# Performance work log

Hardware: AMD Instinct MI355X
Metric: run time of the kernel (lower is better)

Reference implementation:

```python
import jax, jax.numpy as jnp
import numpy as np

B, C, D, N, K = 2, 64, 3, 4096, 16
E = 2 * C      # edge-feature channels (128)
H = 2 * E      # expansion hidden channels (256)


def setup_inputs() -> dict:
    key = jax.random.key(0)
    ks = jax.random.split(key, 7)
    s1 = 1.0 / np.sqrt(E).astype(np.float32)
    s2 = 1.0 / np.sqrt(H).astype(np.float32)
    return {
        "x":  jax.random.normal(ks[0], (B, C, D, N), jnp.float32),
        "W1": jax.random.normal(ks[1], (H, E), jnp.float32) * s1,
        "b1": jax.random.normal(ks[2], (H,), jnp.float32) * s1,
        "W2": jax.random.normal(ks[3], (H, H), jnp.float32) * s2,
        "b2": jax.random.normal(ks[4], (H,), jnp.float32) * s2,
        "W3": jax.random.normal(ks[5], (C, H), jnp.float32) * s2,
        "b3": jax.random.normal(ks[6], (C,), jnp.float32) * s2,
    }


def _knn_idx(pc, k):
    """pc: (B, C, N). Returns (B, k, N) indices of k nearest neighbors
    (self excluded), matching KNN(ref=pc, query=pc) then idx[:, 1:, :]."""
    sq = jnp.sum(pc * pc, axis=1)                                  # (B, N)
    d2 = sq[:, :, None] - 2.0 * jnp.einsum('bcn,bcm->bnm', pc, pc) + sq[:, None, :]
    _, idx = jax.lax.top_k(-d2, k + 1)                             # (B, N, k+1) nearest-first
    return jnp.transpose(idx[:, :, 1:], (0, 2, 1))                 # drop self -> (B, k, N)


def reference(x, W1, b1, W2, b2, W3, b3):
    mean_pc = jnp.mean(x, axis=2)                                  # (B, C, N)
    idx = _knn_idx(mean_pc, K)                                     # (B, K, N), int32
    # grouping_operation: out[b,c,k,n] = mean_pc[b, c, idx[b,k,n]]
    nbr = jax.vmap(lambda f, i: f[:, i])(mean_pc, idx)             # (B, C, K, N)
    central = jnp.broadcast_to(x[:, :, None, :, :], (B, C, K, D, N))
    nbr_e = jnp.broadcast_to(nbr[:, :, :, None, :], (B, C, K, D, N))
    edge = jnp.concatenate([central, nbr_e - central], axis=1)     # (B, 2C, K, D, N)
    bc = lambda b: b[None, :, None, None, None]
    h = jax.nn.relu(jnp.einsum('oi,bikdn->bokdn', W1, edge) + bc(b1))
    h = jax.nn.relu(jnp.einsum('oi,bikdn->bokdn', W2, h) + bc(b2))
    r = jnp.einsum('oi,bikdn->bokdn', W3, h) + bc(b3)              # (B, C, K, D, N)
    return jnp.max(r, axis=2) + x                                  # (B, C, D, N)
```

## Files before the change

kernel.cpp:

```cpp
#include <hip/hip_runtime.h>

typedef unsigned short u16;
typedef float f32x4 __attribute__((ext_vector_type(4)));
typedef short bf16x8 __attribute__((ext_vector_type(8)));
typedef u16 u16x4 __attribute__((ext_vector_type(4)));
typedef unsigned int uint2v __attribute__((ext_vector_type(2)));


static __device__ __forceinline__ u16 f2bf(float x) {
    union { float f; unsigned int u; } v; v.f = x;
    unsigned int u = v.u;
    unsigned int r = u + 0x7fffu + ((u >> 16) & 1u);
    return (u16)(r >> 16);
}

static __device__ __forceinline__ float bf2f(u16 h) {
    union { unsigned int u; float f; } v; v.u = ((unsigned int)h) << 16;
    return v.f;
}

static __device__ __forceinline__ unsigned int pk2(float a, float b) {
    return (unsigned int)f2bf(a) | ((unsigned int)f2bf(b) << 16);
}

__global__ __launch_bounds__(256) void mean_kernel(const float* __restrict__ x,
                                                   float* __restrict__ pc) {
    int t = blockIdx.x * 256 + threadIdx.x;
    int n = t & 4095;
    int bc = t >> 12;
    const float* xp = x + bc * 3 * 4096 + n;
    pc[t] = (xp[0] + xp[4096] + xp[8192]) / 3.0f;
}

__global__ __launch_bounds__(256) void sq_kernel(const float* __restrict__ pc,
                                                 float* __restrict__ sq) {
    int t = blockIdx.x * 256 + threadIdx.x;
    int b = t >> 12, n = t & 4095;
    float s = 0.f;
    #pragma unroll
    for (int c = 0; c < 64; ++c) {
        float v = pc[(b * 64 + c) * 4096 + n];
        s += v * v;
    }
    sq[t] = s;
}

#define INSERT(dist, idxv) do { \
    float _v = (dist); int _vi = (idxv); \
    _Pragma("unroll") \
    for (int _s = 0; _s < 16; ++_s) { \
        bool _c = _v < bd[_s]; \
        float _nb = _c ? _v : bd[_s]; \
        float _nv = _c ? bd[_s] : _v; \
        int _nbi = _c ? _vi : bi[_s]; \
        int _nvi = _c ? bi[_s] : _vi; \
        bd[_s] = _nb; _v = _nv; bi[_s] = _nbi; _vi = _nvi; \
    } } while (0)

__global__ __launch_bounds__(256, 3) void knn_part_kernel(const float* __restrict__ pc,
                                                          const float* __restrict__ sq,
                                                          float* __restrict__ pd,
                                                          int* __restrict__ pi) {
    __shared__ float ptile[64][128];
    __shared__ float sqt[128];
    int tid = threadIdx.x;
    int bid = blockIdx.x;
    int ch = bid & 31, qb = (bid >> 5) & 15, b = bid >> 9;
    int n = qb * 256 + tid;
    int m0 = ch * 128;

    #pragma unroll
    for (int it = 0; it < 8; ++it) {
        int lin4 = it * 256 + tid;
        int c = lin4 >> 5, mm4 = (lin4 & 31) * 4;
        *(float4*)&ptile[c][mm4] =
            *(const float4*)&pc[(b * 64 + c) * 4096 + m0 + mm4];
    }
    if (tid < 128) sqt[tid] = sq[b * 4096 + m0 + tid];

    float qv[64];
    #pragma unroll
    for (int c = 0; c < 64; ++c) qv[c] = pc[(b * 64 + c) * 4096 + n];
    float sqn = sq[b * 4096 + n];

    float bd[16]; int bi[16];
    #pragma unroll
    for (int s = 0; s < 16; ++s) { bd[s] = 3.4e38f; bi[s] = -1; }
    __syncthreads();

    for (int mb = 0; mb < 128; mb += 4) {
        float d0 = 0.f, d1 = 0.f, d2 = 0.f, d3 = 0.f;
        #pragma unroll
        for (int c = 0; c < 64; ++c) {
            float4 pv = *(const float4*)&ptile[c][mb];
            float qc = qv[c];
            d0 = fmaf(qc, pv.x, d0);
            d1 = fmaf(qc, pv.y, d1);
            d2 = fmaf(qc, pv.z, d2);
            d3 = fmaf(qc, pv.w, d3);
        }
        int m = m0 + mb;
        float e0 = (sqn - 2.f * d0) + sqt[mb + 0]; if (m + 0 == n) e0 = 3.4e38f;
        float e1 = (sqn - 2.f * d1) + sqt[mb + 1]; if (m + 1 == n) e1 = 3.4e38f;
        float e2 = (sqn - 2.f * d2) + sqt[mb + 2]; if (m + 2 == n) e2 = 3.4e38f;
        float e3 = (sqn - 2.f * d3) + sqt[mb + 3]; if (m + 3 == n) e3 = 3.4e38f;
        INSERT(e0, m + 0);
        INSERT(e1, m + 1);
        INSERT(e2, m + 2);
        INSERT(e3, m + 3);
    }
    int base = ((b * 4096 + n) * 32 + ch) * 16;
    #pragma unroll
    for (int s = 0; s < 16; ++s) { pd[base + s] = bd[s]; pi[base + s] = bi[s]; }
}

__global__ __launch_bounds__(256) void knn_merge_kernel(const float* __restrict__ pd,
                                                        const int* __restrict__ pi,
                                                        int* __restrict__ idxw) {
    int tid = threadIdx.x;
    int lane = tid & 63;
    int q = blockIdx.x * 4 + (tid >> 6);
    int base = q * 512;

    float d[8]; int ix[8];
    #pragma unroll
    for (int j = 0; j < 8; ++j) {
        d[j] = pd[base + lane + 64 * j];
        ix[j] = pi[base + lane + 64 * j];
    }

    for (int e = 0; e < 16; ++e) {
        float lmd = d[0]; int lmi = ix[0];
        #pragma unroll
        for (int j = 1; j < 8; ++j) {
            bool c = d[j] < lmd;
            lmd = c ? d[j] : lmd;
            lmi = c ? ix[j] : lmi;
        }
        float wm = lmd;
        #pragma unroll
        for (int off = 32; off; off >>= 1)
            wm = fminf(wm, __shfl_xor(wm, off));
        unsigned long long msk = __ballot(lmd == wm);
        int L = (int)__ffsll(msk) - 1;
        int wmi = __shfl(lmi, L);
        if (lane == 0) idxw[q * 16 + e] = wmi;
        if (lane == L) {
            #pragma unroll
            for (int j = 0; j < 8; ++j)
                if (ix[j] == wmi) d[j] = 3.4e38f;
        }
    }
}

__global__ __launch_bounds__(256) void prep_kernel(const float* __restrict__ W1,
                                                   const float* __restrict__ W2,
                                                   const float* __restrict__ W3,
                                                   u16* __restrict__ W2bf,
                                                   u16* __restrict__ W3bf,
                                                   float* __restrict__ W1dT,
                                                   float* __restrict__ W1bT) {
    int t = blockIdx.x * 256 + threadIdx.x;
    W2bf[t] = f2bf(W2[t]);
    if (t < 16384) {
        W3bf[t] = f2bf(W3[t]);
        int c = t >> 8, h = t & 255;
        float wa = W1[h * 128 + c];
        float wb = W1[h * 128 + 64 + c];
        W1dT[t] = wa - wb;
        W1bT[t] = wb;
    }
}

__global__ __launch_bounds__(256) void q_kernel(const float* __restrict__ pc,
                                               const float* __restrict__ W1bT,
                                               u16* __restrict__ Qbf) {
    int h = threadIdx.x;
    int bid = blockIdx.x;
    int b = bid >> 10, m0 = (bid & 1023) * 4;
    float a0 = 0.f, a1 = 0.f, a2 = 0.f, a3 = 0.f;
    for (int c = 0; c < 64; ++c) {
        float w = W1bT[c * 256 + h];
        float4 pv = *(const float4*)(pc + (b * 64 + c) * 4096 + m0);
        a0 = fmaf(w, pv.x, a0);
        a1 = fmaf(w, pv.y, a1);
        a2 = fmaf(w, pv.z, a2);
        a3 = fmaf(w, pv.w, a3);
    }
    int ob = (b * 4096 + m0) * 256 + h;
    Qbf[ob] = f2bf(a0); Qbf[ob + 256] = f2bf(a1);
    Qbf[ob + 512] = f2bf(a2); Qbf[ob + 768] = f2bf(a3);
}

__global__ __launch_bounds__(256) void p_kernel(const float* __restrict__ x,
                                               const float* __restrict__ W1dT,
                                               const float* __restrict__ b1,
                                               u16* __restrict__ Pbf) {
    int h = threadIdx.x;
    int bid = blockIdx.x;
    int b = bid / 3072;
    int rem = bid % 3072;
    int d = rem >> 10;
    int n0 = (rem & 1023) * 4;
    float bias = b1[h];
    float a0 = bias, a1 = bias, a2 = bias, a3 = bias;
    for (int c = 0; c < 64; ++c) {
        float w = W1dT[c * 256 + h];
        float4 xv = *(const float4*)(x + ((b * 64 + c) * 3 + d) * 4096 + n0);
        a0 = fmaf(w, xv.x, a0);
        a1 = fmaf(w, xv.y, a1);
        a2 = fmaf(w, xv.z, a2);
        a3 = fmaf(w, xv.w, a3);
    }
    int ob = ((b * 3 + d) * 4096 + n0) * 256 + h;
    Pbf[ob] = f2bf(a0); Pbf[ob + 256] = f2bf(a1);
    Pbf[ob + 512] = f2bf(a2); Pbf[ob + 768] = f2bf(a3);
}

__global__ __launch_bounds__(256) void fused_mlp_kernel(const float* __restrict__ x,
                                                        const u16* __restrict__ Pbf,
                                                        const u16* __restrict__ Qbf,
                                                        const int* __restrict__ idxw,
                                                        const u16* __restrict__ W2bf,
                                                        const u16* __restrict__ W3bf,
                                                        const float* __restrict__ b2,
                                                        const float* __restrict__ b3,
                                                        float* __restrict__ out) {
    __shared__ u16 hL[96][264];

    int tid = threadIdx.x;
    int bid = blockIdx.x;
    int b = bid >> 11;
    int n0 = (bid & 2047) * 2;

    int w = tid >> 6, lane = tid & 63;

    {
        int g = w & 1, kh = (w >> 1) * 8;
        int n = n0 + g;
        u16x4 pv[3];
        #pragma unroll
        for (int d = 0; d < 3; ++d)
            pv[d] = *(const u16x4*)&Pbf[((b * 3 + d) * 4096 + n) * 256 + lane * 4];
        const int* idq = idxw + (b * 4096 + n) * 16 + kh;
        #pragma unroll
        for (int kk = 0; kk < 8; ++kk) {
            int m = idq[kk];
            u16x4 qv = *(const u16x4*)&Qbf[(b * 4096 + m) * 256 + lane * 4];
            float q0 = bf2f(qv[0]), q1 = bf2f(qv[1]), q2 = bf2f(qv[2]), q3 = bf2f(qv[3]);
            #pragma unroll
            for (int d = 0; d < 3; ++d) {
                uint2v hv;
                hv[0] = pk2(fmaxf(bf2f(pv[d][0]) + q0, 0.f), fmaxf(bf2f(pv[d][1]) + q1, 0.f));
                hv[1] = pk2(fmaxf(bf2f(pv[d][2]) + q2, 0.f), fmaxf(bf2f(pv[d][3]) + q3, 0.f));
                *(uint2v*)&hL[g * 48 + d * 16 + kh + kk][lane * 4] = hv;
            }
        }
    }
    __syncthreads();

    int cl = lane & 15, q = lane >> 4;

    f32x4 acc[4][6];
    #pragma unroll
    for (int i = 0; i < 4; ++i)
        #pragma unroll
        for (int jt = 0; jt < 6; ++jt)
            acc[i][jt] = (f32x4){0.f, 0.f, 0.f, 0.f};

    const u16* Arow = W2bf + (w * 64 + cl) * 256 + q * 8;
    for (int kt = 0; kt < 8; ++kt) {
        int k0 = kt * 32;
        bf16x8 a[4], bb[6];
        #pragma unroll
        for (int i = 0; i < 4; ++i)
            a[i] = *(const bf16x8*)(Arow + i * 4096 + k0);
        #pragma unroll
        for (int jt = 0; jt < 6; ++jt)
            bb[jt] = *(const bf16x8*)(&hL[jt * 16 + cl][k0 + q * 8]);
        #pragma unroll
        for (int i = 0; i < 4; ++i)
            #pragma unroll
            for (int jt = 0; jt < 6; ++jt)
                acc[i][jt] = __builtin_amdgcn_mfma_f32_16x16x32_bf16(a[i], bb[jt], acc[i][jt], 0, 0, 0);
    }
    __syncthreads();

    #pragma unroll
    for (int i = 0; i < 4; ++i) {
        int rowb = w * 64 + i * 16 + q * 4;
        float4 bv = *(const float4*)(b2 + rowb);
        #pragma unroll
        for (int jt = 0; jt < 6; ++jt) {
            f32x4 v = acc[i][jt];
            uint2v hv;
            hv[0] = pk2(fmaxf(v[0] + bv.x, 0.f), fmaxf(v[1] + bv.y, 0.f));
            hv[1] = pk2(fmaxf(v[2] + bv.z, 0.f), fmaxf(v[3] + bv.w, 0.f));
            *(uint2v*)&hL[jt * 16 + cl][rowb] = hv;
        }
    }
    __syncthreads();

    f32x4 acc3[6];
    #pragma unroll
    for (int jt = 0; jt < 6; ++jt) acc3[jt] = (f32x4){0.f, 0.f, 0.f, 0.f};

    const u16* A3row = W3bf + (w * 16 + cl) * 256 + q * 8;
    for (int kt = 0; kt < 8; ++kt) {
        int k0 = kt * 32;
        bf16x8 a3 = *(const bf16x8*)(A3row + k0);
        #pragma unroll
        for (int jt = 0; jt < 6; ++jt) {
            bf16x8 bb = *(const bf16x8*)(&hL[jt * 16 + cl][k0 + q * 8]);
            acc3[jt] = __builtin_amdgcn_mfma_f32_16x16x32_bf16(a3, bb, acc3[jt], 0, 0, 0);
        }
    }

    int rowb = w * 16 + q * 4;
    float4 b3v = *(const float4*)(b3 + rowb);
    #pragma unroll
    for (int jt = 0; jt < 6; ++jt) {
        int g = jt / 3, d = jt % 3;
        int n = n0 + g;
        f32x4 v = acc3[jt];
        v[0] += b3v.x;
        v[1] += b3v.y;
        v[2] += b3v.z;
        v[3] += b3v.w;
        #pragma unroll
        for (int off = 1; off < 16; off <<= 1) {
            v[0] = fmaxf(v[0], __shfl_xor(v[0], off));
            v[1] = fmaxf(v[1], __shfl_xor(v[1], off));
            v[2] = fmaxf(v[2], __shfl_xor(v[2], off));
            v[3] = fmaxf(v[3], __shfl_xor(v[3], off));
        }
        if (cl == 0) {
            #pragma unroll
            for (int r = 0; r < 4; ++r) {
                int addr = ((b * 64 + rowb + r) * 3 + d) * 4096 + n;
                out[addr] = v[r] + x[addr];
            }
        }
    }
}

extern "C" void kernel_launch(void* const* d_in, const int* in_sizes, int n_in,
                              void* d_out, int out_size, void* d_ws, size_t ws_size,
                              hipStream_t stream) {
    (void)in_sizes; (void)n_in; (void)out_size; (void)ws_size;
    const float* x  = (const float*)d_in[0];
    const float* W1 = (const float*)d_in[1];
    const float* b1 = (const float*)d_in[2];
    const float* W2 = (const float*)d_in[3];
    const float* b2 = (const float*)d_in[4];
    const float* W3 = (const float*)d_in[5];
    const float* b3 = (const float*)d_in[6];
    float* out = (float*)d_out;

    char* ws = (char*)d_ws;
    float* pc   = (float*)(ws + 0);
    float* sq   = (float*)(ws + 2097152);
    int*   idxw = (int*)  (ws + 2129920);
    u16*   Qbf  = (u16*)  (ws + 2654208);
    u16*   Pbf  = (u16*)  (ws + 6848512);
    u16*   W2bf = (u16*)  (ws + 19431424);
    u16*   W3bf = (u16*)  (ws + 19562496);
    float* W1dT = (float*)(ws + 19595264);
    float* W1bT = (float*)(ws + 19660800);
    float* pd   = (float*)(ws + 2654208);
    int*   pi   = (int*)  (ws + 19726336);

    mean_kernel<<<2048, 256, 0, stream>>>(x, pc);
    sq_kernel<<<32, 256, 0, stream>>>(pc, sq);
    knn_part_kernel<<<1024, 256, 0, stream>>>(pc, sq, pd, pi);
    knn_merge_kernel<<<2048, 256, 0, stream>>>(pd, pi, idxw);
    prep_kernel<<<256, 256, 0, stream>>>(W1, W2, W3, W2bf, W3bf, W1dT, W1bT);
    q_kernel<<<2048, 256, 0, stream>>>(pc, W1bT, Qbf);
    p_kernel<<<6144, 256, 0, stream>>>(x, W1dT, b1, Pbf);
    fused_mlp_kernel<<<4096, 256, 0, stream>>>(x, Pbf, Qbf, idxw, W2bf, W3bf, b2, b3, out);
}
```

Before: 379.0 us.

## Fuse weight prep into mean kernel, widen P/Q kernels, halve fused MLP LDS

Weight conversion moves into mean_kernel, which removes one launch. The q and p kernels now compute 8 points per block instead of 4, halving their grid sizes. fused_mlp_kernel processes its two points one after another, so the shared buffer shrinks to 48 rows and the accumulators halve. It also declares 4 waves-per-EU launch bounds to raise occupancy. In exchange, the W2/W3 fragments are reloaded per point and extra barriers are added.

```diff
diff --git a/kernel.cpp b/kernel.cpp
--- a/kernel.cpp
+++ b/kernel.cpp
@@ -5,6 +5,7 @@
 typedef short bf16x8 __attribute__((ext_vector_type(8)));
 typedef u16 u16x4 __attribute__((ext_vector_type(4)));
 typedef unsigned int uint2v __attribute__((ext_vector_type(2)));
+typedef unsigned int uint4v __attribute__((ext_vector_type(4)));
 
 
 static __device__ __forceinline__ u16 f2bf(float x) {
@@ -24,12 +25,31 @@
 }
 
 __global__ __launch_bounds__(256) void mean_kernel(const float* __restrict__ x,
-                                                   float* __restrict__ pc) {
+                                                   float* __restrict__ pc,
+                                                   const float* __restrict__ W1,
+                                                   const float* __restrict__ W2,
+                                                   const float* __restrict__ W3,
+                                                   u16* __restrict__ W2bf,
+                                                   u16* __restrict__ W3bf,
+                                                   float* __restrict__ W1dT,
+                                                   float* __restrict__ W1bT) {
     int t = blockIdx.x * 256 + threadIdx.x;
     int n = t & 4095;
     int bc = t >> 12;
     const float* xp = x + bc * 3 * 4096 + n;
     pc[t] = (xp[0] + xp[4096] + xp[8192]) / 3.0f;
+
+    if (t < 65536) {
+        W2bf[t] = f2bf(W2[t]);
+        if (t < 16384) {
+            W3bf[t] = f2bf(W3[t]);
+            int c = t >> 8, h = t & 255;
+            float wa = W1[h * 128 + c];
+            float wb = W1[h * 128 + 64 + c];
+            W1dT[t] = wa - wb;
+            W1bT[t] = wb;
+        }
+    }
 }
 
 __global__ __launch_bounds__(256) void sq_kernel(const float* __restrict__ pc,
@@ -153,43 +173,29 @@
     }
 }
 
-__global__ __launch_bounds__(256) void prep_kernel(const float* __restrict__ W1,
-                                                   const float* __restrict__ W2,
-                                                   const float* __restrict__ W3,
-                                                   u16* __restrict__ W2bf,
-                                                   u16* __restrict__ W3bf,
-                                                   float* __restrict__ W1dT,
-                                                   float* __restrict__ W1bT) {
-    int t = blockIdx.x * 256 + threadIdx.x;
-    W2bf[t] = f2bf(W2[t]);
-    if (t < 16384) {
-        W3bf[t] = f2bf(W3[t]);
-        int c = t >> 8, h = t & 255;
-        float wa = W1[h * 128 + c];
-        float wb = W1[h * 128 + 64 + c];
-        W1dT[t] = wa - wb;
-        W1bT[t] = wb;
-    }
-}
-
 __global__ __launch_bounds__(256) void q_kernel(const float* __restrict__ pc,
                                                const float* __restrict__ W1bT,
                                                u16* __restrict__ Qbf) {
     int h = threadIdx.x;
     int bid = blockIdx.x;
-    int b = bid >> 10, m0 = (bid & 1023) * 4;
+    int b = bid >> 9, m0 = (bid & 511) * 8;
     float a0 = 0.f, a1 = 0.f, a2 = 0.f, a3 = 0.f;
+    float a4 = 0.f, a5 = 0.f, a6 = 0.f, a7 = 0.f;
     for (int c = 0; c < 64; ++c) {
         float w = W1bT[c * 256 + h];
-        float4 pv = *(const float4*)(pc + (b * 64 + c) * 4096 + m0);
-        a0 = fmaf(w, pv.x, a0);
-        a1 = fmaf(w, pv.y, a1);
-        a2 = fmaf(w, pv.z, a2);
-        a3 = fmaf(w, pv.w, a3);
+        const float* pr = pc + (b * 64 + c) * 4096 + m0;
+        float4 p0 = *(const float4*)pr;
+        float4 p1 = *(const float4*)(pr + 4);
+        a0 = fmaf(w, p0.x, a0); a1 = fmaf(w, p0.y, a1);
+        a2 = fmaf(w, p0.z, a2); a3 = fmaf(w, p0.w, a3);
+        a4 = fmaf(w, p1.x, a4); a5 = fmaf(w, p1.y, a5);
+        a6 = fmaf(w, p1.z, a6); a7 = fmaf(w, p1.w, a7);
     }
     int ob = (b * 4096 + m0) * 256 + h;
     Qbf[ob] = f2bf(a0); Qbf[ob + 256] = f2bf(a1);
     Qbf[ob + 512] = f2bf(a2); Qbf[ob + 768] = f2bf(a3);
+    Qbf[ob + 1024] = f2bf(a4); Qbf[ob + 1280] = f2bf(a5);
+    Qbf[ob + 1536] = f2bf(a6); Qbf[ob + 1792] = f2bf(a7);
 }
 
 __global__ __launch_bounds__(256) void p_kernel(const float* __restrict__ x,
@@ -198,35 +204,40 @@
                                                u16* __restrict__ Pbf) {
     int h = threadIdx.x;
     int bid = blockIdx.x;
-    int b = bid / 3072;
-    int rem = bid % 3072;
-    int d = rem >> 10;
-    int n0 = (rem & 1023) * 4;
+    int b = bid / 1536;
+    int rem = bid % 1536;
+    int d = rem >> 9;
+    int n0 = (rem & 511) * 8;
     float bias = b1[h];
     float a0 = bias, a1 = bias, a2 = bias, a3 = bias;
+    float a4 = bias, a5 = bias, a6 = bias, a7 = bias;
     for (int c = 0; c < 64; ++c) {
         float w = W1dT[c * 256 + h];
-        float4 xv = *(const float4*)(x + ((b * 64 + c) * 3 + d) * 4096 + n0);
-        a0 = fmaf(w, xv.x, a0);
-        a1 = fmaf(w, xv.y, a1);
-        a2 = fmaf(w, xv.z, a2);
-        a3 = fmaf(w, xv.w, a3);
+        const float* xr = x + ((b * 64 + c) * 3 + d) * 4096 + n0;
+        float4 x0 = *(const float4*)xr;
+        float4 x1 = *(const float4*)(xr + 4);
+        a0 = fmaf(w, x0.x, a0); a1 = fmaf(w, x0.y, a1);
+        a2 = fmaf(w, x0.z, a2); a3 = fmaf(w, x0.w, a3);
+        a4 = fmaf(w, x1.x, a4); a5 = fmaf(w, x1.y, a5);
+        a6 = fmaf(w, x1.z, a6); a7 = fmaf(w, x1.w, a7);
     }
     int ob = ((b * 3 + d) * 4096 + n0) * 256 + h;
     Pbf[ob] = f2bf(a0); Pbf[ob + 256] = f2bf(a1);
     Pbf[ob + 512] = f2bf(a2); Pbf[ob + 768] = f2bf(a3);
-}
-
-__global__ __launch_bounds__(256) void fused_mlp_kernel(const float* __restrict__ x,
-                                                        const u16* __restrict__ Pbf,
-                                                        const u16* __restrict__ Qbf,
-                                                        const int* __restrict__ idxw,
-                                                        const u16* __restrict__ W2bf,
-                                                        const u16* __restrict__ W3bf,
-                                                        const float* __restrict__ b2,
-                                                        const float* __restrict__ b3,
-                                                        float* __restrict__ out) {
-    __shared__ u16 hL[96][264];
+    Pbf[ob + 1024] = f2bf(a4); Pbf[ob + 1280] = f2bf(a5);
+    Pbf[ob + 1536] = f2bf(a6); Pbf[ob + 1792] = f2bf(a7);
+}
+
+__global__ __launch_bounds__(256, 4) void fused_mlp_kernel(const float* __restrict__ x,
+                                                           const u16* __restrict__ Pbf,
+                                                           const u16* __restrict__ Qbf,
+                                                           const int* __restrict__ idxw,
+                                                           const u16* __restrict__ W2bf,
+                                                           const u16* __restrict__ W3bf,
+                                                           const float* __restrict__ b2,
+                                                           const float* __restrict__ b3,
+                                                           float* __restrict__ out) {
+    __shared__ u16 hL[48][264];
 
     int tid = threadIdx.x;
     int bid = blockIdx.x;
@@ -234,113 +245,125 @@
     int n0 = (bid & 2047) * 2;
 
     int w = tid >> 6, lane = tid & 63;
-
-    {
-        int g = w & 1, kh = (w >> 1) * 8;
-        int n = n0 + g;
-        u16x4 pv[3];
-        #pragma unroll
-        for (int d = 0; d < 3; ++d)
-            pv[d] = *(const u16x4*)&Pbf[((b * 3 + d) * 4096 + n) * 256 + lane * 4];
-        const int* idq = idxw + (b * 4096 + n) * 16 + kh;
-        #pragma unroll
-        for (int kk = 0; kk < 8; ++kk) {
-            int m = idq[kk];
-            u16x4 qv = *(const u16x4*)&Qbf[(b * 4096 + m) * 256 + lane * 4];
-            float q0 = bf2f(qv[0]), q1 = bf2f(qv[1]), q2 = bf2f(qv[2]), q3 = bf2f(qv[3]);
+    int cl = lane & 15, q = lane >> 4;
+    int r = lane >> 5, l32 = lane & 31;
+
+    const u16* Arow = W2bf + (w * 64 + cl) * 256 + q * 8;
+    const u16* A3row = W3bf + (w * 16 + cl) * 256 + q * 8;
+
+    #pragma unroll 1
+    for (int pp = 0; pp < 2; ++pp) {
+        int n = n0 + pp;
+
+        {
+            float pf[3][8];
             #pragma unroll
             for (int d = 0; d < 3; ++d) {
+                bf16x8 pv8 = *(const bf16x8*)&Pbf[((b * 3 + d) * 4096 + n) * 256 + l32 * 8];
+                #pragma unroll
+                for (int j = 0; j < 8; ++j) pf[d][j] = bf2f((u16)pv8[j]);
+            }
+            const int* idq = idxw + (b * 4096 + n) * 16;
+            #pragma unroll
+            for (int pr = 0; pr < 2; ++pr) {
+                int kk = (w << 2) + (pr << 1) + r;
+                int m = idq[kk];
+                bf16x8 qv8 = *(const bf16x8*)&Qbf[(b * 4096 + m) * 256 + l32 * 8];
+                float qf[8];
+                #pragma unroll
+                for (int j = 0; j < 8; ++j) qf[j] = bf2f((u16)qv8[j]);
+                #pragma unroll
+                for (int d = 0; d < 3; ++d) {
+                    uint4v hv;
+                    hv[0] = pk2(fmaxf(pf[d][0] + qf[0], 0.f), fmaxf(pf[d][1] + qf[1], 0.f));
+                    hv[1] = pk2(fmaxf(pf[d][2] + qf[2], 0.f), fmaxf(pf[d][3] + qf[3], 0.f));
+                    hv[2] = pk2(fmaxf(pf[d][4] + qf[4], 0.f), fmaxf(pf[d][5] + qf[5], 0.f));
+                    hv[3] = pk2(fmaxf(pf[d][6] + qf[6], 0.f), fmaxf(pf[d][7] + qf[7], 0.f));
+                    *(uint4v*)&hL[d * 16 + kk][l32 * 8] = hv;
+                }
+            }
+        }
+        __syncthreads();
+
+        f32x4 acc[4][3];
+        #pragma unroll
+        for (int i = 0; i < 4; ++i)
+            #pragma unroll
+            for (int jt = 0; jt < 3; ++jt)
+                acc[i][jt] = (f32x4){0.f, 0.f, 0.f, 0.f};
+
+        for (int kt = 0; kt < 8; ++kt) {
+            int k0 = kt * 32;
+            bf16x8 a[4], bb[3];
+            #pragma unroll
+            for (int i = 0; i < 4; ++i)
+                a[i] = *(const bf16x8*)(Arow + i * 4096 + k0);
+            #pragma unroll
+            for (int jt = 0; jt < 3; ++jt)
+                bb[jt] = *(const bf16x8*)(&hL[jt * 16 + cl][k0 + q * 8]);
+            #pragma unroll
+            for (int i = 0; i < 4; ++i)
+                #pragma unroll
+                for (int jt = 0; jt < 3; ++jt)
+                    acc[i][jt] = __builtin_amdgcn_mfma_f32_16x16x32_bf16(a[i], bb[jt], acc[i][jt], 0, 0, 0);
+        }
+        __syncthreads();
+
+        #pragma unroll
+        for (int i = 0; i < 4; ++i) {
+            int rowb = w * 64 + i * 16 + q * 4;
+            float4 bv = *(const float4*)(b2 + rowb);
+            #pragma unroll
+            for (int jt = 0; jt < 3; ++jt) {
+                f32x4 v = acc[i][jt];
                 uint2v hv;
-                hv[0] = pk2(fmaxf(bf2f(pv[d][0]) + q0, 0.f), fmaxf(bf2f(pv[d][1]) + q1, 0.f));
-                hv[1] = pk2(fmaxf(bf2f(pv[d][2]) + q2, 0.f), fmaxf(bf2f(pv[d][3]) + q3, 0.f));
-                *(uint2v*)&hL[g * 48 + d * 16 + kh + kk][lane * 4] = hv;
-            }
-        }
-    }
-    __syncthreads();
-
-    int cl = lane & 15, q = lane >> 4;
-
-    f32x4 acc[4][6];
-    #pragma unroll
-    for (int i = 0; i < 4; ++i)
-        #pragma unroll
-        for (int jt = 0; jt < 6; ++jt)
-            acc[i][jt] = (f32x4){0.f, 0.f, 0.f, 0.f};
-
-    const u16* Arow = W2bf + (w * 64 + cl) * 256 + q * 8;
-    for (int kt = 0; kt < 8; ++kt) {
-        int k0 = kt * 32;
-        bf16x8 a[4], bb[6];
-        #pragma unroll
-        for (int i = 0; i < 4; ++i)
-            a[i] = *(const bf16x8*)(Arow + i * 4096 + k0);
-        #pragma unroll
-        for (int jt = 0; jt < 6; ++jt)
-            bb[jt] = *(const bf16x8*)(&hL[jt * 16 + cl][k0 + q * 8]);
-        #pragma unroll
-        for (int i = 0; i < 4; ++i)
-            #pragma unroll
-            for (int jt = 0; jt < 6; ++jt)
-                acc[i][jt] = __builtin_amdgcn_mfma_f32_16x16x32_bf16(a[i], bb[jt], acc[i][jt], 0, 0, 0);
-    }
-    __syncthreads();
-
-    #pragma unroll
-    for (int i = 0; i < 4; ++i) {
-        int rowb = w * 64 + i * 16 + q * 4;
-        float4 bv = *(const float4*)(b2 + rowb);
-        #pragma unroll
-        for (int jt = 0; jt < 6; ++jt) {
-            f32x4 v = acc[i][jt];
-            uint2v hv;
-            hv[0] = pk2(fmaxf(v[0] + bv.x, 0.f), fmaxf(v[1] + bv.y, 0.f));
-            hv[1] = pk2(fmaxf(v[2] + bv.z, 0.f), fmaxf(v[3] + bv.w, 0.f));
-            *(uint2v*)&hL[jt * 16 + cl][rowb] = hv;
-        }
-    }
-    __syncthreads();
-
-    f32x4 acc3[6];
-    #pragma unroll
-    for (int jt = 0; jt < 6; ++jt) acc3[jt] = (f32x4){0.f, 0.f, 0.f, 0.f};
-
-    const u16* A3row = W3bf + (w * 16 + cl) * 256 + q * 8;
-    for (int kt = 0; kt < 8; ++kt) {
-        int k0 = kt * 32;
-        bf16x8 a3 = *(const bf16x8*)(A3row + k0);
-        #pragma unroll
-        for (int jt = 0; jt < 6; ++jt) {
-            bf16x8 bb = *(const bf16x8*)(&hL[jt * 16 + cl][k0 + q * 8]);
-            acc3[jt] = __builtin_amdgcn_mfma_f32_16x16x32_bf16(a3, bb, acc3[jt], 0, 0, 0);
-        }
-    }
-
-    int rowb = w * 16 + q * 4;
-    float4 b3v = *(const float4*)(b3 + rowb);
-    #pragma unroll
-    for (int jt = 0; jt < 6; ++jt) {
-        int g = jt / 3, d = jt % 3;
-        int n = n0 + g;
-        f32x4 v = acc3[jt];
-        v[0] += b3v.x;
-        v[1] += b3v.y;
-        v[2] += b3v.z;
-        v[3] += b3v.w;
-        #pragma unroll
-        for (int off = 1; off < 16; off <<= 1) {
-            v[0] = fmaxf(v[0], __shfl_xor(v[0], off));
-            v[1] = fmaxf(v[1], __shfl_xor(v[1], off));
-            v[2] = fmaxf(v[2], __shfl_xor(v[2], off));
-            v[3] = fmaxf(v[3], __shfl_xor(v[3], off));
-        }
-        if (cl == 0) {
-            #pragma unroll
-            for (int r = 0; r < 4; ++r) {
-                int addr = ((b * 64 + rowb + r) * 3 + d) * 4096 + n;
-                out[addr] = v[r] + x[addr];
-            }
-        }
+                hv[0] = pk2(fmaxf(v[0] + bv.x, 0.f), fmaxf(v[1] + bv.y, 0.f));
+                hv[1] = pk2(fmaxf(v[2] + bv.z, 0.f), fmaxf(v[3] + bv.w, 0.f));
+                *(uint2v*)&hL[jt * 16 + cl][rowb] = hv;
+            }
+        }
+        __syncthreads();
+
+        f32x4 acc3[3];
+        #pragma unroll
+        for (int jt = 0; jt < 3; ++jt) acc3[jt] = (f32x4){0.f, 0.f, 0.f, 0.f};
+
+        for (int kt = 0; kt < 8; ++kt) {
+            int k0 = kt * 32;
+            bf16x8 a3 = *(const bf16x8*)(A3row + k0);
+            #pragma unroll
+            for (int jt = 0; jt < 3; ++jt) {
+                bf16x8 bb = *(const bf16x8*)(&hL[jt * 16 + cl][k0 + q * 8]);
+                acc3[jt] = __builtin_amdgcn_mfma_f32_16x16x32_bf16(a3, bb, acc3[jt], 0, 0, 0);
+            }
+        }
+
+        int rowb = w * 16 + q * 4;
+        float4 b3v = *(const float4*)(b3 + rowb);
+        #pragma unroll
+        for (int jt = 0; jt < 3; ++jt) {
+            int d = jt;
+            f32x4 v = acc3[jt];
+            v[0] += b3v.x;
+            v[1] += b3v.y;
+            v[2] += b3v.z;
+            v[3] += b3v.w;
+            #pragma unroll
+            for (int off = 1; off < 16; off <<= 1) {
+                v[0] = fmaxf(v[0], __shfl_xor(v[0], off));
+                v[1] = fmaxf(v[1], __shfl_xor(v[1], off));
+                v[2] = fmaxf(v[2], __shfl_xor(v[2], off));
+                v[3] = fmaxf(v[3], __shfl_xor(v[3], off));
+            }
+            if (cl == 0) {
+                #pragma unroll
+                for (int rr = 0; rr < 4; ++rr) {
+                    int addr = ((b * 64 + rowb + rr) * 3 + d) * 4096 + n;
+                    out[addr] = v[rr] + x[addr];
+                }
+            }
+        }
+        __syncthreads();
     }
 }
 
@@ -370,12 +393,11 @@
     float* pd   = (float*)(ws + 2654208);
     int*   pi   = (int*)  (ws + 19726336);
 
-    mean_kernel<<<2048, 256, 0, stream>>>(x, pc);
+    mean_kernel<<<2048, 256, 0, stream>>>(x, pc, W1, W2, W3, W2bf, W3bf, W1dT, W1bT);
     sq_kernel<<<32, 256, 0, stream>>>(pc, sq);
     knn_part_kernel<<<1024, 256, 0, stream>>>(pc, sq, pd, pi);
     knn_merge_kernel<<<2048, 256, 0, stream>>>(pd, pi, idxw);
-    prep_kernel<<<256, 256, 0, stream>>>(W1, W2, W3, W2bf, W3bf, W1dT, W1bT);
-    q_kernel<<<2048, 256, 0, stream>>>(pc, W1bT, Qbf);
-    p_kernel<<<6144, 256, 0, stream>>>(x, W1dT, b1, Pbf);
+    q_kernel<<<1024, 256, 0, stream>>>(pc, W1bT, Qbf);
+    p_kernel<<<3072, 256, 0, stream>>>(x, W1dT, b1, Pbf);
     fused_mlp_kernel<<<4096, 256, 0, stream>>>(x, Pbf, Qbf, idxw, W2bf, W3bf, b2, b3, out);
 }
```

After: 546.9 us. +44.3%, slower.
